# Optimization experiments

Hardware: AMD Instinct MI355X
Metric: run time of the kernel (lower is better)

Reference implementation:

```python
import jax, jax.numpy as jnp
import numpy as np

STATE_LEN = 128
SEQ_LEN = 2048  # middle segment length; total T = SEQ_LEN + 2*STATE_LEN = 2304


def _l2norm(t):
    # matches torch F.normalize(p=2, dim=-1, eps=1e-12)
    n = jnp.sqrt(jnp.sum(t * t, axis=-1, keepdims=True))
    return t / jnp.maximum(n, 1e-12)


def setup_inputs() -> dict:
    key = jax.random.key(0)
    ks = jax.random.split(key, 8)
    B, D, H, dk, dv = 1, 1024, 16, 64, 64
    T = SEQ_LEN + 2 * STATE_LEN
    x = jax.random.normal(ks[0], (B, T, D), dtype=jnp.float32)
    w = lambda k, do: jax.random.normal(k, (H, D, do), dtype=jnp.float32) * 0.02
    return {
        "x": x,
        "Wq": w(ks[1], dk),
        "Wk": w(ks[2], dk),
        "Wv": w(ks[3], dv),
        "Wq_state": w(ks[4], dk),
        "Wk_state": w(ks[5], dk),
        "Wv_state": w(ks[6], dv),
        "scaling_factor": jnp.full((H,), 1.0 / np.sqrt(dk), dtype=jnp.float32),
    }


def reference(x, Wq, Wk, Wv, Wq_state, Wk_state, Wv_state, scaling_factor):
    sl, seq = STATE_LEN, SEQ_LEN
    # extract_state: [start_state | sequence | end_state]
    x0 = x[:, :sl]
    xm = x[:, sl:sl + seq]
    x1 = x[:, sl + seq:]

    proj = lambda t, W: jnp.einsum('bsd,hdk->bhsk', t, W)  # StackedLinear, no bias

    q = jnp.concatenate([_l2norm(proj(x0, Wq_state)), _l2norm(proj(xm, Wq)), _l2norm(proj(x1, Wq_state))], axis=2)
    k = jnp.concatenate([_l2norm(proj(x0, Wk_state)), _l2norm(proj(xm, Wk)), _l2norm(proj(x1, Wk_state))], axis=2)
    v = jnp.concatenate([_l2norm(proj(x0, Wv_state)), _l2norm(proj(xm, Wv)), _l2norm(proj(x1, Wv_state))], axis=2)

    T = q.shape[2]
    row = jnp.arange(T)[:, None]
    col = jnp.arange(T)[None, :]
    allowed = col <= row  # causal (tril, diagonal=0)
    # end-state rows may not attend to start-state cols (attn_bias[..., seq+sl:seq+2sl, :sl] = 0 before log)
    allowed = allowed & ~((row >= sl + seq) & (col < sl))
    mask = jnp.where(allowed, 0.0, -jnp.inf).astype(q.dtype)  # log of 0/1 tril

    # per-head learnable scale applied to q@k^T, then additive mask, softmax, @v
    scores = jnp.einsum('bhqd,bhkd->bhqk', q, k) * scaling_factor[None, :, None, None] + mask
    att = jax.nn.softmax(scores, axis=-1)
    return jnp.einsum('bhqk,bhkd->bhqd', att, v)
```

## Files before the change

### kernel.cpp

```cpp
#include <hip/hip_runtime.h>
#include <hip/hip_bf16.h>

#define T_TOT 2304
#define DDIM  1024
#define NH    16
#define DK    64
#define SLEN  128
#define SEQ   2048

typedef __bf16 bf16x8 __attribute__((ext_vector_type(8)));
typedef __bf16 bf16x4 __attribute__((ext_vector_type(4)));
typedef float  f32x4  __attribute__((ext_vector_type(4)));

__device__ __forceinline__ void async_copy16(const void* gsrc, void* ldst) {
  __builtin_amdgcn_global_load_lds(
      (const __attribute__((address_space(1))) void*)gsrc,
      (__attribute__((address_space(3))) void*)ldst, 16, 0, 0);
}

__device__ __forceinline__ void lds_barrier() {
  __asm__ volatile("s_waitcnt lgkmcnt(0)\n\ts_barrier" ::: "memory");
}

__global__ __launch_bounds__(256) void convert_kernel(
    const float* __restrict__ x,
    const float* __restrict__ Wq, const float* __restrict__ Wk,
    const float* __restrict__ Wv, const float* __restrict__ Wqs,
    const float* __restrict__ Wks, const float* __restrict__ Wvs,
    __bf16* __restrict__ xb, __bf16* __restrict__ Wt) {
  const int b = blockIdx.x;
  const int tid = threadIdx.x;
  if (b < 576) {
    const float4* xin = (const float4*)x;
#pragma unroll
    for (int it = 0; it < 4; ++it) {
      int idx4 = b * 1024 + it * 256 + tid;
      float4 v = xin[idx4];
      bf16x4 o;
      o[0] = (__bf16)v.x; o[1] = (__bf16)v.y; o[2] = (__bf16)v.z; o[3] = (__bf16)v.w;
      *(bf16x4*)(xb + (size_t)idx4 * 4) = o;
    }
    return;
  }
  __shared__ float tile[64 * 65];
  const int wb = b - 576;
  const int m  = wb >> 8;
  const int rem = wb & 255;
  const int h  = rem >> 4;
  const int dt = rem & 15;
  const int d0 = dt * 64;
  const float* Wsrc = (m == 0 ? Wq : m == 1 ? Wk : m == 2 ? Wv
                      : m == 3 ? Wqs : m == 4 ? Wks : Wvs) + (size_t)h * (DDIM * DK);
#pragma unroll
  for (int rr = 0; rr < 4; ++rr) {
    int drow = rr * 16 + (tid >> 4);
    int nc   = (tid & 15) * 4;
    float4 v = *(const float4*)(Wsrc + (size_t)(d0 + drow) * DK + nc);
    tile[(nc + 0) * 65 + drow] = v.x;
    tile[(nc + 1) * 65 + drow] = v.y;
    tile[(nc + 2) * 65 + drow] = v.z;
    tile[(nc + 3) * 65 + drow] = v.w;
  }
  __syncthreads();
  {
    int n  = tid >> 2;
    int rg = (tid & 3) * 16;
    __bf16* dst = Wt + (((size_t)(m * NH + h)) * DK + n) * DDIM + d0 + rg;
    bf16x8 o0, o1;
#pragma unroll
    for (int e = 0; e < 8; e++) o0[e] = (__bf16)tile[n * 65 + rg + e];
#pragma unroll
    for (int e = 0; e < 8; e++) o1[e] = (__bf16)tile[n * 65 + rg + 8 + e];
    *(bf16x8*)dst = o0;
    *(bf16x8*)(dst + 8) = o1;
  }
}

__global__ __launch_bounds__(256) void proj_kernel(
    const __bf16* __restrict__ xb, const __bf16* __restrict__ Wt,
    const float* __restrict__ scal,
    __bf16* __restrict__ qkv, __bf16* __restrict__ vt) {
  const int ntile = blockIdx.x;
  const int rt    = blockIdx.y;
  const int which = blockIdx.z;
  const int r0    = rt * 64;
  const int m     = (rt < 2 || rt >= 34) ? which + 3 : which;

  __shared__ __bf16 Xs[64 * 64];
  __shared__ __bf16 Wsh[128 * 64];

  const int tid  = threadIdx.x;
  const int wave = tid >> 6, lane = tid & 63;
  const int quad = lane >> 4, lc = lane & 15;
  const int wr   = wave >> 1, wc = wave & 1;
  const int h    = ntile * 2 + wc;

  const __bf16* Wbase = Wt + ((size_t)m * NH) * (DK * DDIM) + (size_t)(ntile * 128) * DDIM;

  const f32x4 fz = {0.f, 0.f, 0.f, 0.f};
  f32x4 acc[2][4];
#pragma unroll
  for (int i = 0; i < 2; i++)
#pragma unroll
    for (int j = 0; j < 4; j++) acc[i][j] = fz;

  for (int k0 = 0; k0 < DDIM; k0 += 64) {
#pragma unroll
    for (int it = 0; it < 2; ++it) {
      int L = it * 256 + tid;
      int row = L >> 3, c = (L & 7) ^ (row & 7);
      async_copy16(xb + (size_t)(r0 + row) * DDIM + k0 + c * 8,
                   (char*)Xs + (size_t)(it * 256 + wave * 64) * 16);
    }
#pragma unroll
    for (int it = 0; it < 4; ++it) {
      int L = it * 256 + tid;
      int row = L >> 3, c = (L & 7) ^ (row & 7);
      async_copy16(Wbase + (size_t)row * DDIM + k0 + c * 8,
                   (char*)Wsh + (size_t)(it * 256 + wave * 64) * 16);
    }
    __syncthreads();
#pragma unroll
    for (int kk = 0; kk < 2; kk++) {
      bf16x8 afr[2], bfr[4];
#pragma unroll
      for (int i = 0; i < 2; i++) {
        int row = wr * 32 + i * 16 + lc;
        int ch  = (kk * 4 + quad) ^ (row & 7);
        afr[i] = *(const bf16x8*)(Xs + (row * 8 + ch) * 8);
      }
#pragma unroll
      for (int j = 0; j < 4; j++) {
        int row = wc * 64 + j * 16 + lc;
        int ch  = (kk * 4 + quad) ^ (row & 7);
        bfr[j] = *(const bf16x8*)(Wsh + (row * 8 + ch) * 8);
      }
#pragma unroll
      for (int i = 0; i < 2; i++)
#pragma unroll
        for (int j = 0; j < 4; j++)
          acc[i][j] = __builtin_amdgcn_mfma_f32_16x16x32_bf16(afr[i], bfr[j], acc[i][j], 0, 0, 0);
    }
    __syncthreads();
  }

  const float qscale = (which == 0) ? scal[h] * 1.44269504088896f : 1.0f;
  float inv4[2][4];
#pragma unroll
  for (int i = 0; i < 2; i++) {
#pragma unroll
    for (int r = 0; r < 4; r++) {
      float s = 0.f;
#pragma unroll
      for (int j = 0; j < 4; j++) { float v = acc[i][j][r]; s += v * v; }
#pragma unroll
      for (int off = 1; off < 16; off <<= 1) s += __shfl_xor(s, off, 64);
      inv4[i][r] = qscale / fmaxf(sqrtf(s), 1e-12f);
    }
  }
  if (which == 2) {
    __bf16* vtp = vt + (size_t)h * (DK * T_TOT);
#pragma unroll
    for (int i = 0; i < 2; i++) {
      int rowbase = r0 + wr * 32 + i * 16 + quad * 4;
#pragma unroll
      for (int j = 0; j < 4; j++) {
        bf16x4 o;
#pragma unroll
        for (int r = 0; r < 4; r++) o[r] = (__bf16)(acc[i][j][r] * inv4[i][r]);
        *(bf16x4*)(vtp + (size_t)(j * 16 + lc) * T_TOT + rowbase) = o;
      }
    }
  } else {
    __bf16* outp = qkv + ((size_t)(which * NH + h)) * ((size_t)T_TOT * DK);
#pragma unroll
    for (int i = 0; i < 2; i++)
#pragma unroll
      for (int r = 0; r < 4; r++) {
        int row = r0 + wr * 32 + i * 16 + quad * 4 + r;
#pragma unroll
        for (int j = 0; j < 4; j++)
          outp[(size_t)row * DK + j * 16 + lc] = (__bf16)(acc[i][j][r] * inv4[i][r]);
      }
  }
}

__global__ __launch_bounds__(256, 3) void attn_kernel(
    const __bf16* __restrict__ qkv, const __bf16* __restrict__ vt,
    float* __restrict__ Opart, float* __restrict__ Lpart) {
  const int b    = blockIdx.x;
  const int h    = b & 15;
  const int rest = b >> 4;
  const int qg   = 35 - (rest >> 1);
  const int si   = rest & 1;
  const int q0b  = qg * 64;
  const int tid  = threadIdx.x;
  const int wave = tid >> 6, lane = tid & 63;
  const int quad = lane >> 4, lc = lane & 15;

  const __bf16* qp = qkv + ((size_t)h) * ((size_t)T_TOT * DK);
  const __bf16* kp = qkv + ((size_t)(NH + h)) * ((size_t)T_TOT * DK);
  const __bf16* vp = vt + (size_t)h * (DK * T_TOT);

  __shared__ __align__(16) char smem[40960];
  __bf16* Ks = (__bf16*)smem;
  __bf16* Vs = (__bf16*)(smem + 16384);
  __bf16* Pw = (__bf16*)(smem + 32768) + wave * 1024;

  bf16x8 qf[2];
#pragma unroll
  for (int kk = 0; kk < 2; kk++)
    qf[kk] = *(const bf16x8*)(qp + (size_t)(q0b + wave * 16 + lc) * DK + kk * 32 + quad * 8);

  const f32x4 fz = {0.f, 0.f, 0.f, 0.f};
  f32x4 acc[4];
#pragma unroll
  for (int dt = 0; dt < 4; dt++) acc[dt] = fz;
  float lp = 0.f;

  const int jsAll = (q0b >= SLEN + SEQ) ? 2 : 0;
  const int n     = qg - jsAll + 1;
  const int half  = (n + 1) >> 1;
  const int j0    = jsAll + (si ? half : 0);
  const int j1    = si ? qg : (jsAll + half - 1);

  auto stage = [&](int j, int bufi) {
    const __bf16* kT = kp + (size_t)j * 64 * DK;
    __bf16* Kd = Ks + bufi * 4096;
    __bf16* Vd = Vs + bufi * 4096;
#pragma unroll
    for (int it = 0; it < 2; ++it) {
      int L = it * 256 + tid;
      int row = L >> 3, c = (L & 7) ^ (row & 7);
      async_copy16(kT + (size_t)row * DK + c * 8,
                   (char*)Kd + (size_t)(it * 256 + wave * 64) * 16);
    }
#pragma unroll
    for (int it = 0; it < 2; ++it) {
      int L = it * 256 + tid;
      int d = L >> 3, c = (L & 7) ^ (d & 7);
      async_copy16(vp + (size_t)d * T_TOT + j * 64 + c * 8,
                   (char*)Vd + (size_t)(it * 256 + wave * 64) * 16);
    }
  };

  int cur = 0;
  if (j0 <= j1) stage(j0, 0);

  for (int j = j0; j <= j1; ++j) {
    __syncthreads();
    if (j < j1) stage(j + 1, cur ^ 1);

    const __bf16* Kc = Ks + cur * 4096;
    const __bf16* Vc = Vs + cur * 4096;

    f32x4 s[4];
#pragma unroll
    for (int kvt = 0; kvt < 4; kvt++) {
      int row = kvt * 16 + lc;
      bf16x8 a0 = *(const bf16x8*)(Kc + (row * 8 + (quad ^ (lc & 7))) * 8);
      bf16x8 a1 = *(const bf16x8*)(Kc + (row * 8 + ((4 + quad) ^ (lc & 7))) * 8);
      f32x4 t = __builtin_amdgcn_mfma_f32_16x16x32_bf16(a0, qf[0], fz, 0, 0, 0);
      s[kvt]  = __builtin_amdgcn_mfma_f32_16x16x32_bf16(a1, qf[1], t, 0, 0, 0);
    }

    const bool diag = (j == qg);
#pragma unroll
    for (int kvt = 0; kvt < 4; kvt++) {
      if (diag) {
#pragma unroll
        for (int r = 0; r < 4; r++)
          if ((kvt * 16 + quad * 4 + r) > (wave * 16 + lc)) s[kvt][r] = -__builtin_inff();
      }
      bf16x4 pb;
#pragma unroll
      for (int r = 0; r < 4; r++) {
        float pe = exp2f(s[kvt][r]);
        lp += pe;
        pb[r] = (__bf16)pe;
      }
      int c = (kvt * 4 + quad) ^ ((lc & 7) << 1);
      *(bf16x4*)(Pw + lc * 64 + c * 4) = pb;
    }

    bf16x8 pB[2];
#pragma unroll
    for (int kk = 0; kk < 2; kk++)
      pB[kk] = *(const bf16x8*)(Pw + lc * 64 + ((kk * 8 + quad * 2) ^ ((lc & 7) << 1)) * 4);
#pragma unroll
    for (int dt = 0; dt < 4; dt++) {
      int row = dt * 16 + lc;
#pragma unroll
      for (int kk = 0; kk < 2; kk++) {
        bf16x8 vA = *(const bf16x8*)(Vc + (row * 8 + ((kk * 4 + quad) ^ (lc & 7))) * 8);
        acc[dt] = __builtin_amdgcn_mfma_f32_16x16x32_bf16(vA, pB[kk], acc[dt], 0, 0, 0);
      }
    }
    cur ^= 1;
  }

  lp += __shfl_xor(lp, 16, 64);
  lp += __shfl_xor(lp, 32, 64);
  if (lane < 16) Lpart[(size_t)b * 64 + wave * 16 + lane] = lp;

  __syncthreads();
  float* Ot = (float*)smem + wave * (16 * 68);
#pragma unroll
  for (int dt = 0; dt < 4; dt++)
#pragma unroll
    for (int r = 0; r < 4; r++)
      Ot[lc * 68 + dt * 16 + quad * 4 + r] = acc[dt][r];

  float* Ob = Opart + (size_t)b * 4096;
  const int q2 = lane >> 2, dsg = (lane & 3) * 16;
#pragma unroll
  for (int g = 0; g < 4; g++) {
    f32x4 v = *(const f32x4*)(&Ot[q2 * 68 + dsg + g * 4]);
    *(f32x4*)(&Ob[(size_t)(wave * 16 + q2) * 64 + dsg + g * 4]) = v;
  }
}

__global__ __launch_bounds__(256) void combine_kernel(
    const float* __restrict__ Opart, const float* __restrict__ Lpart,
    float* __restrict__ out) {
  const int b  = blockIdx.x;
  const int h  = b & 15;
  const int qg = b >> 4;
  const int b0 = (((35 - qg) * 2) << 4) | h;
  const int b1 = b0 + 16;
  const int tid = threadIdx.x;

  __shared__ float invl[64];
  if (tid < 64)
    invl[tid] = 1.0f / (Lpart[(size_t)b0 * 64 + tid] + Lpart[(size_t)b1 * 64 + tid]);
  __syncthreads();

  const float* O0 = Opart + (size_t)b0 * 4096;
  const float* O1 = Opart + (size_t)b1 * 4096;
  float* op = out + ((size_t)h * T_TOT + qg * 64) * DK;
#pragma unroll
  for (int it = 0; it < 4; ++it) {
    int i4 = it * 256 + tid;
    f32x4 a = *(const f32x4*)(&O0[i4 * 4]);
    f32x4 c = *(const f32x4*)(&O1[i4 * 4]);
    float iv = invl[i4 >> 4];
    f32x4 o;
#pragma unroll
    for (int r = 0; r < 4; r++) o[r] = (a[r] + c[r]) * iv;
    *(f32x4*)(&op[i4 * 4]) = o;
  }
}

extern "C" void kernel_launch(void* const* d_in, const int* in_sizes, int n_in,
                              void* d_out, int out_size, void* d_ws, size_t ws_size,
                              hipStream_t stream) {
  const float* x    = (const float*)d_in[0];
  const float* Wq   = (const float*)d_in[1];
  const float* Wk   = (const float*)d_in[2];
  const float* Wv   = (const float*)d_in[3];
  const float* Wqs  = (const float*)d_in[4];
  const float* Wks  = (const float*)d_in[5];
  const float* Wvs  = (const float*)d_in[6];
  const float* scal = (const float*)d_in[7];
  float* out = (float*)d_out;

  char* ws = (char*)d_ws;
  size_t off = 0;
  __bf16* xb    = (__bf16*)(ws + off); off += (size_t)T_TOT * DDIM * 2;
  __bf16* Wt    = (__bf16*)(ws + off); off += (size_t)6 * NH * DK * DDIM * 2;
  __bf16* qkv   = (__bf16*)(ws + off); off += (size_t)2 * NH * T_TOT * DK * 2;
  __bf16* vt    = (__bf16*)(ws + off); off += (size_t)NH * DK * T_TOT * 2;
  float*  Opart = (float*)(ws + off);  off += (size_t)1152 * 4096 * 4;
  float*  Lpart = (float*)(ws + off);

  convert_kernel<<<2112, 256, 0, stream>>>(x, Wq, Wk, Wv, Wqs, Wks, Wvs, xb, Wt);
  proj_kernel<<<dim3(8, 36, 3), 256, 0, stream>>>(xb, Wt, scal, qkv, vt);
  attn_kernel<<<dim3(1152), 256, 0, stream>>>(qkv, vt, Opart, Lpart);
  combine_kernel<<<dim3(576), 256, 0, stream>>>(Opart, Lpart, out);
}
```

Baseline: 142.1 us.

## Fuse split-KV combine into attention via atomic last-block counter; add MFMA setprio

Removes the separate combine kernel launch. Each attention block now increments a per-(query group, head) atomic counter after writing its partial output, and the second block to finish merges both partials and writes the normalized result. The counters are zeroed in the convert kernel. The change also raises wave priority around the two MFMA sections to favour matrix-core issue. This saves one launch and its tail, at the cost of threadfences, an atomic per block and some extra work in the late-finishing blocks.

```diff
diff --git a/kernel.cpp b/kernel.cpp
--- a/kernel.cpp
+++ b/kernel.cpp
@@ -18,19 +18,17 @@
       (__attribute__((address_space(3))) void*)ldst, 16, 0, 0);
 }
 
-__device__ __forceinline__ void lds_barrier() {
-  __asm__ volatile("s_waitcnt lgkmcnt(0)\n\ts_barrier" ::: "memory");
-}
-
 __global__ __launch_bounds__(256) void convert_kernel(
     const float* __restrict__ x,
     const float* __restrict__ Wq, const float* __restrict__ Wk,
     const float* __restrict__ Wv, const float* __restrict__ Wqs,
     const float* __restrict__ Wks, const float* __restrict__ Wvs,
-    __bf16* __restrict__ xb, __bf16* __restrict__ Wt) {
+    __bf16* __restrict__ xb, __bf16* __restrict__ Wt, int* __restrict__ cnt) {
   const int b = blockIdx.x;
   const int tid = threadIdx.x;
   if (b < 576) {
+    if (b == 0)
+      for (int i = tid; i < 576; i += 256) cnt[i] = 0;
     const float4* xin = (const float4*)x;
 #pragma unroll
     for (int it = 0; it < 4; ++it) {
@@ -187,7 +185,8 @@
 
 __global__ __launch_bounds__(256, 3) void attn_kernel(
     const __bf16* __restrict__ qkv, const __bf16* __restrict__ vt,
-    float* __restrict__ Opart, float* __restrict__ Lpart) {
+    float* __restrict__ Opart, float* __restrict__ Lpart,
+    int* __restrict__ cnt, float* __restrict__ out) {
   const int b    = blockIdx.x;
   const int h    = b & 15;
   const int rest = b >> 4;
@@ -203,6 +202,7 @@
   const __bf16* vp = vt + (size_t)h * (DK * T_TOT);
 
   __shared__ __align__(16) char smem[40960];
+  __shared__ int lastFlag;
   __bf16* Ks = (__bf16*)smem;
   __bf16* Vs = (__bf16*)(smem + 16384);
   __bf16* Pw = (__bf16*)(smem + 32768) + wave * 1024;
@@ -255,6 +255,7 @@
     const __bf16* Vc = Vs + cur * 4096;
 
     f32x4 s[4];
+    __builtin_amdgcn_s_setprio(1);
 #pragma unroll
     for (int kvt = 0; kvt < 4; kvt++) {
       int row = kvt * 16 + lc;
@@ -263,6 +264,7 @@
       f32x4 t = __builtin_amdgcn_mfma_f32_16x16x32_bf16(a0, qf[0], fz, 0, 0, 0);
       s[kvt]  = __builtin_amdgcn_mfma_f32_16x16x32_bf16(a1, qf[1], t, 0, 0, 0);
     }
+    __builtin_amdgcn_s_setprio(0);
 
     const bool diag = (j == qg);
 #pragma unroll
@@ -287,6 +289,7 @@
 #pragma unroll
     for (int kk = 0; kk < 2; kk++)
       pB[kk] = *(const bf16x8*)(Pw + lc * 64 + ((kk * 8 + quad * 2) ^ ((lc & 7) << 1)) * 4);
+    __builtin_amdgcn_s_setprio(1);
 #pragma unroll
     for (int dt = 0; dt < 4; dt++) {
       int row = dt * 16 + lc;
@@ -296,6 +299,7 @@
         acc[dt] = __builtin_amdgcn_mfma_f32_16x16x32_bf16(vA, pB[kk], acc[dt], 0, 0, 0);
       }
     }
+    __builtin_amdgcn_s_setprio(0);
     cur ^= 1;
   }
 
@@ -318,36 +322,34 @@
     f32x4 v = *(const f32x4*)(&Ot[q2 * 68 + dsg + g * 4]);
     *(f32x4*)(&Ob[(size_t)(wave * 16 + q2) * 64 + dsg + g * 4]) = v;
   }
-}
-
-__global__ __launch_bounds__(256) void combine_kernel(
-    const float* __restrict__ Opart, const float* __restrict__ Lpart,
-    float* __restrict__ out) {
-  const int b  = blockIdx.x;
-  const int h  = b & 15;
-  const int qg = b >> 4;
+
+  __threadfence();
+  __syncthreads();
+  if (tid == 0) lastFlag = (atomicAdd(&cnt[qg * 16 + h], 1) == 1);
+  __syncthreads();
+  if (!lastFlag) return;
+  __threadfence();
+
   const int b0 = (((35 - qg) * 2) << 4) | h;
   const int b1 = b0 + 16;
-  const int tid = threadIdx.x;
-
-  __shared__ float invl[64];
+  float* invl = (float*)smem;
   if (tid < 64)
     invl[tid] = 1.0f / (Lpart[(size_t)b0 * 64 + tid] + Lpart[(size_t)b1 * 64 + tid]);
   __syncthreads();
 
   const float* O0 = Opart + (size_t)b0 * 4096;
   const float* O1 = Opart + (size_t)b1 * 4096;
-  float* op = out + ((size_t)h * T_TOT + qg * 64) * DK;
+  float* op = out + ((size_t)h * T_TOT + q0b) * DK;
 #pragma unroll
   for (int it = 0; it < 4; ++it) {
     int i4 = it * 256 + tid;
-    f32x4 a = *(const f32x4*)(&O0[i4 * 4]);
-    f32x4 c = *(const f32x4*)(&O1[i4 * 4]);
+    f32x4 a = *(const f32x4*)(&O0[(size_t)i4 * 4]);
+    f32x4 c = *(const f32x4*)(&O1[(size_t)i4 * 4]);
     float iv = invl[i4 >> 4];
     f32x4 o;
 #pragma unroll
     for (int r = 0; r < 4; r++) o[r] = (a[r] + c[r]) * iv;
-    *(f32x4*)(&op[i4 * 4]) = o;
+    *(f32x4*)(&op[(size_t)i4 * 4]) = o;
   }
 }
 
@@ -371,10 +373,10 @@
   __bf16* qkv   = (__bf16*)(ws + off); off += (size_t)2 * NH * T_TOT * DK * 2;
   __bf16* vt    = (__bf16*)(ws + off); off += (size_t)NH * DK * T_TOT * 2;
   float*  Opart = (float*)(ws + off);  off += (size_t)1152 * 4096 * 4;
-  float*  Lpart = (float*)(ws + off);
-
-  convert_kernel<<<2112, 256, 0, stream>>>(x, Wq, Wk, Wv, Wqs, Wks, Wvs, xb, Wt);
+  float*  Lpart = (float*)(ws + off);  off += (size_t)1152 * 64 * 4;
+  int*    cnt   = (int*)(ws + off);    off += (size_t)576 * 4;
+
+  convert_kernel<<<2112, 256, 0, stream>>>(x, Wq, Wk, Wv, Wqs, Wks, Wvs, xb, Wt, cnt);
   proj_kernel<<<dim3(8, 36, 3), 256, 0, stream>>>(xb, Wt, scal, qkv, vt);
-  attn_kernel<<<dim3(1152), 256, 0, stream>>>(qkv, vt, Opart, Lpart);
-  combine_kernel<<<dim3(576), 256, 0, stream>>>(Opart, Lpart, out);
-}
+  attn_kernel<<<dim3(1152), 256, 0, stream>>>(qkv, vt, Opart, Lpart, cnt, out);
+}
```

Result: slower. 378.0 us (+166.0%).
